# Performance work log

Hardware: AMD Instinct MI355X
Metric: run time of the kernel (lower is better)

The kernel has to match this reference:

```python
import jax, jax.numpy as jnp
import numpy as np


def setup_inputs() -> dict:
    key = jax.random.key(0)
    k1, k2, k3 = jax.random.split(key, 3)
    B, T1, T2, D = 16, 1024, 1024, 256
    x = jax.random.normal(k1, (B, T1, D), dtype=jnp.float32)
    y = jax.random.normal(k2, (B, T2, D), dtype=jnp.float32)
    WS = jax.random.normal(k3, (3 * D,), dtype=jnp.float32) * 0.05
    return {"x": x, "y": y, "WS": WS}


def reference(x, y, WS):
    # BiDAF trilinear similarity. Original computes
    #   S[b,i,j] = sum_k concat([x_i, 1, x_i])_k * concat([1, y_j, y_j])_k * WS_k
    # which decomposes exactly into:
    #   S = x @ w1 (broadcast over j) + y @ w2 (broadcast over i) + (x * w3) @ y^T
    D = x.shape[-1]
    w1, w2, w3 = WS[:D], WS[D:2 * D], WS[2 * D:]
    term_x = jnp.einsum('bid,d->bi', x, w1)            # [B, T1]
    term_y = jnp.einsum('bjd,d->bj', y, w2)            # [B, T2]
    term_xy = jnp.einsum('bid,bjd->bij', x * w3, y)    # [B, T1, T2]
    return term_xy + term_x[:, :, None] + term_y[:, None, :]
```

## Files before the change

### kernel.cpp

```cpp
#include <hip/hip_runtime.h>

#define DK 256
#define TT 1024
#define NB 16

typedef __attribute__((ext_vector_type(8))) short bf16x8;
typedef __attribute__((ext_vector_type(4))) float f32x4;

__device__ __forceinline__ unsigned int cvt_pk_bf16(float lo, float hi) {
    unsigned int r;
    asm("v_cvt_pk_bf16_f32 %0, %1, %2" : "=v"(r) : "v"(lo), "v"(hi));
    return r;
}

union BF8 { uint4 u; bf16x8 v; };

__global__ __launch_bounds__(512, 4) void fused_kernel(
    const float* __restrict__ x, const float* __restrict__ y,
    const float* __restrict__ WS, float* __restrict__ out)
{
    __shared__ unsigned short Bs[128 * DK];
    __shared__ float tys[128];

    const int tid  = threadIdx.x;
    const int lane = tid & 63;
    const int w    = tid >> 6;

    const int id = blockIdx.x;
    const int b  = id & 15;
    const int is = (id >> 4) & 3;
    const int jt = id >> 6;

    {
        const float* gY0 = y + ((size_t)b * TT + jt * 128) * DK;
        const int c = tid & 31;
        const float* w3p = WS + 2 * DK + c * 8;
        const float* w2p = WS + DK + c * 8;
        const float4 wa = *(const float4*)(w3p);
        const float4 wb = *(const float4*)(w3p + 4);
        const float4 va = *(const float4*)(w2p);
        const float4 vb = *(const float4*)(w2p + 4);
        #pragma unroll
        for (int it = 0; it < 8; ++it) {
            const int j = it * 16 + (tid >> 5);
            const float* gY = gY0 + (size_t)j * DK + c * 8;
            const float4 ya = *(const float4*)(gY);
            const float4 yb = *(const float4*)(gY + 4);
            float p = ya.x * va.x + ya.y * va.y + ya.z * va.z + ya.w * va.w
                    + yb.x * vb.x + yb.y * vb.y + yb.z * vb.z + yb.w * vb.w;
            uint4 o;
            o.x = cvt_pk_bf16(ya.x * wa.x, ya.y * wa.y);
            o.y = cvt_pk_bf16(ya.z * wa.z, ya.w * wa.w);
            o.z = cvt_pk_bf16(yb.x * wb.x, yb.y * wb.y);
            o.w = cvt_pk_bf16(yb.z * wb.z, yb.w * wb.w);
            const int slot = c ^ (j & 7);
            *(uint4*)(Bs + j * DK + slot * 8) = o;
            p += __shfl_xor(p, 1);
            p += __shfl_xor(p, 2);
            p += __shfl_xor(p, 4);
            p += __shfl_xor(p, 8);
            p += __shfl_xor(p, 16);
            if ((tid & 31) == 0) tys[j] = p;
        }
    }
    __syncthreads();

    const int mfr  = lane & 15;
    const int quad = lane >> 4;
    const int i0   = is * 256 + w * 32;
    const float* gA = x + ((size_t)b * TT + i0) * DK;

    f32x4 acc[2][8];
    #pragma unroll
    for (int it = 0; it < 2; ++it)
        #pragma unroll
        for (int n = 0; n < 8; ++n)
            acc[it][n] = (f32x4){0.f, 0.f, 0.f, 0.f};
    float txp[2] = {0.f, 0.f};

    #pragma unroll
    for (int ks = 0; ks < 8; ++ks) {
        const float* w1p = WS + ks * 32 + quad * 8;
        const float4 w1a = *(const float4*)(w1p);
        const float4 w1b = *(const float4*)(w1p + 4);
        bf16x8 av[2];
        #pragma unroll
        for (int it = 0; it < 2; ++it) {
            const float* rp = gA + (size_t)(it * 16 + mfr) * DK
                              + ks * 32 + quad * 8;
            const float4 xa = *(const float4*)rp;
            const float4 xb = *(const float4*)(rp + 4);
            txp[it] += xa.x * w1a.x + xa.y * w1a.y + xa.z * w1a.z + xa.w * w1a.w
                     + xb.x * w1b.x + xb.y * w1b.y + xb.z * w1b.z + xb.w * w1b.w;
            BF8 cv;
            cv.u.x = cvt_pk_bf16(xa.x, xa.y);
            cv.u.y = cvt_pk_bf16(xa.z, xa.w);
            cv.u.z = cvt_pk_bf16(xb.x, xb.y);
            cv.u.w = cvt_pk_bf16(xb.z, xb.w);
            av[it] = cv.v;
        }
        #pragma unroll
        for (int n = 0; n < 8; ++n) {
            const int j    = n * 16 + mfr;
            const int slot = (ks * 4 + quad) ^ (j & 7);
            const bf16x8 bv = *(const bf16x8*)(Bs + j * DK + slot * 8);
            #pragma unroll
            for (int it = 0; it < 2; ++it)
                acc[it][n] = __builtin_amdgcn_mfma_f32_16x16x32_bf16(
                    av[it], bv, acc[it][n], 0, 0, 0);
        }
    }

    #pragma unroll
    for (int it = 0; it < 2; ++it) {
        txp[it] += __shfl_xor(txp[it], 16);
        txp[it] += __shfl_xor(txp[it], 32);
    }

    float tyv[8];
    #pragma unroll
    for (int n = 0; n < 8; ++n)
        tyv[n] = tys[n * 16 + mfr];

    float* outB = out + ((size_t)b << 20) + (size_t)i0 * TT + jt * 128;
    #pragma unroll
    for (int it = 0; it < 2; ++it) {
        #pragma unroll
        for (int r = 0; r < 4; ++r) {
            const int row = it * 16 + quad * 4 + r;
            const float trow = __shfl(txp[it], (lane & 48) | (quad * 4 + r));
            #pragma unroll
            for (int n = 0; n < 8; ++n)
                outB[(size_t)row * TT + n * 16 + mfr] =
                    acc[it][n][r] + trow + tyv[n];
        }
    }
}

extern "C" void kernel_launch(void* const* d_in, const int* in_sizes, int n_in,
                              void* d_out, int out_size, void* d_ws, size_t ws_size,
                              hipStream_t stream)
{
    const float* x  = (const float*)d_in[0];
    const float* y  = (const float*)d_in[1];
    const float* WS = (const float*)d_in[2];
    float* out = (float*)d_out;
    (void)d_ws; (void)ws_size;

    fused_kernel<<<dim3(512), dim3(512), 0, stream>>>(x, y, WS, out);
}
```

Measured before the change: 109.6 us.

## Stage x tiles in LDS with double-buffered async global-to-LDS loads

Each block's 256-row x slab is now staged through a double-buffered LDS area using async global_load_lds in 32-column K slices with an XOR swizzle. The next slice is prefetched while MFMAs run on the current one, in place of direct per-lane global loads of x. This adds 64KB of LDS and a block-wide barrier per K step, and lowers the launch-bounds occupancy hint from 4 to 2. With about 128KB of LDS per block, fewer blocks can be resident per CU, which may offset the gain from the overlap.

```diff
diff --git a/kernel.cpp b/kernel.cpp
--- a/kernel.cpp
+++ b/kernel.cpp
@@ -15,11 +15,12 @@
 
 union BF8 { uint4 u; bf16x8 v; };
 
-__global__ __launch_bounds__(512, 4) void fused_kernel(
+__global__ __launch_bounds__(512, 2) void fused_kernel(
     const float* __restrict__ x, const float* __restrict__ y,
     const float* __restrict__ WS, float* __restrict__ out)
 {
     __shared__ unsigned short Bs[128 * DK];
+    __shared__ float Xp[2][256 * 32];
     __shared__ float tys[128];
 
     const int tid  = threadIdx.x;
@@ -30,6 +31,26 @@
     const int b  = id & 15;
     const int is = (id >> 4) & 3;
     const int jt = id >> 6;
+
+    const int i0blk = is * 256;
+    const float* gX = x + ((size_t)b * TT + i0blk) * DK;
+
+    const int r_ln = lane >> 3;
+    const int c_ln = lane & 7;
+
+    {
+        #pragma unroll
+        for (int t = 0; t < 4; ++t) {
+            const int q = w * 4 + t;
+            const int r = q * 8 + r_ln;
+            const int gc = c_ln ^ (r & 7);
+            const float* gp = gX + (size_t)r * DK + gc * 4;
+            float* lp = &Xp[0][q * 256];
+            __builtin_amdgcn_global_load_lds(
+                (const __attribute__((address_space(1))) void*)gp,
+                (__attribute__((address_space(3))) void*)lp, 16, 0, 0);
+        }
+    }
 
     {
         const float* gY0 = y + ((size_t)b * TT + jt * 128) * DK;
@@ -67,8 +88,8 @@
 
     const int mfr  = lane & 15;
     const int quad = lane >> 4;
-    const int i0   = is * 256 + w * 32;
-    const float* gA = x + ((size_t)b * TT + i0) * DK;
+    const int Rl0  = w * 32 + mfr;
+    const int Rl1  = Rl0 + 16;
 
     f32x4 acc[2][8];
     #pragma unroll
@@ -80,16 +101,32 @@
 
     #pragma unroll
     for (int ks = 0; ks < 8; ++ks) {
+        if (ks < 7) {
+            #pragma unroll
+            for (int t = 0; t < 4; ++t) {
+                const int q = w * 4 + t;
+                const int r = q * 8 + r_ln;
+                const int gc = c_ln ^ (r & 7);
+                const float* gp = gX + (size_t)r * DK + (ks + 1) * 32 + gc * 4;
+                float* lp = &Xp[(ks + 1) & 1][q * 256];
+                __builtin_amdgcn_global_load_lds(
+                    (const __attribute__((address_space(1))) void*)gp,
+                    (__attribute__((address_space(3))) void*)lp, 16, 0, 0);
+            }
+        }
+
         const float* w1p = WS + ks * 32 + quad * 8;
         const float4 w1a = *(const float4*)(w1p);
         const float4 w1b = *(const float4*)(w1p + 4);
         bf16x8 av[2];
+        const int Rl[2] = {Rl0, Rl1};
         #pragma unroll
         for (int it = 0; it < 2; ++it) {
-            const float* rp = gA + (size_t)(it * 16 + mfr) * DK
-                              + ks * 32 + quad * 8;
-            const float4 xa = *(const float4*)rp;
-            const float4 xb = *(const float4*)(rp + 4);
+            const float* pr = &Xp[ks & 1][Rl[it] * 32];
+            const int s0 = (quad * 2) ^ (Rl[it] & 7);
+            const int s1 = (quad * 2 + 1) ^ (Rl[it] & 7);
+            const float4 xa = *(const float4*)(pr + s0 * 4);
+            const float4 xb = *(const float4*)(pr + s1 * 4);
             txp[it] += xa.x * w1a.x + xa.y * w1a.y + xa.z * w1a.z + xa.w * w1a.w
                      + xb.x * w1b.x + xb.y * w1b.y + xb.z * w1b.z + xb.w * w1b.w;
             BF8 cv;
@@ -109,6 +146,8 @@
                 acc[it][n] = __builtin_amdgcn_mfma_f32_16x16x32_bf16(
                     av[it], bv, acc[it][n], 0, 0, 0);
         }
+
+        if (ks < 7) __syncthreads();
     }
 
     #pragma unroll
@@ -122,6 +161,7 @@
     for (int n = 0; n < 8; ++n)
         tyv[n] = tys[n * 16 + mfr];
 
+    const int i0 = i0blk + w * 32;
     float* outB = out + ((size_t)b << 20) + (size_t)i0 * TT + jt * 128;
     #pragma unroll
     for (int it = 0; it < 2; ++it) {
```

New measurement: 126.1 us. +15.1%, slower.

## Split into bf16 prep kernel and GEMM kernel reading precomputed operands

Applied to the files above, without the earlier changes.

Adds a prep kernel that converts x and y (scaled by w3) to bf16 in workspace and computes the per-row x·w1 and y·w2 projections. A separate GEMM kernel then loads bf16 operands and precomputed bias terms instead of re-reading fp32 inputs and reconverting them in every tile. The fused kernel is kept as a fallback when the workspace is too small. This trades an extra launch and a workspace write/read pass for halved operand traffic and less conversion work in the main kernel.

```diff
diff --git a/kernel.cpp b/kernel.cpp
--- a/kernel.cpp
+++ b/kernel.cpp
@@ -14,6 +14,134 @@
 }
 
 union BF8 { uint4 u; bf16x8 v; };
+
+
+__global__ __launch_bounds__(256) void prep_kernel(
+    const float* __restrict__ x, const float* __restrict__ y,
+    const float* __restrict__ WS,
+    unsigned short* __restrict__ xb, unsigned short* __restrict__ yb,
+    float* __restrict__ tx, float* __restrict__ ty)
+{
+    const int lane = threadIdx.x & 63;
+    const int gw   = blockIdx.x * 4 + (threadIdx.x >> 6);
+    const int r    = gw & 16383;
+    const bool isx = gw < 16384;
+
+    const float* src = (isx ? x : y) + (size_t)r * DK + lane * 4;
+    const float4 v  = *(const float4*)src;
+    const float4 wd = *(const float4*)(WS + (isx ? 0 : DK) + lane * 4);
+
+    float dot = v.x * wd.x + v.y * wd.y + v.z * wd.z + v.w * wd.w;
+    dot += __shfl_xor(dot, 1);
+    dot += __shfl_xor(dot, 2);
+    dot += __shfl_xor(dot, 4);
+    dot += __shfl_xor(dot, 8);
+    dot += __shfl_xor(dot, 16);
+    dot += __shfl_xor(dot, 32);
+
+    float4 s = v;
+    if (!isx) {
+        const float4 w3 = *(const float4*)(WS + 2 * DK + lane * 4);
+        s.x = v.x * w3.x; s.y = v.y * w3.y; s.z = v.z * w3.z; s.w = v.w * w3.w;
+    }
+    uint2 o;
+    o.x = cvt_pk_bf16(s.x, s.y);
+    o.y = cvt_pk_bf16(s.z, s.w);
+    unsigned short* dst = (isx ? xb : yb) + (size_t)r * DK + lane * 4;
+    *(uint2*)dst = o;
+    if (lane == 0) (isx ? tx : ty)[r] = dot;
+}
+
+__global__ __launch_bounds__(512, 4) void gemm_kernel(
+    const unsigned short* __restrict__ xb, const unsigned short* __restrict__ yb,
+    const float* __restrict__ tx, const float* __restrict__ ty,
+    float* __restrict__ out)
+{
+    __shared__ unsigned short Bs[128 * DK];
+    __shared__ float txs[256];
+    __shared__ float tys[128];
+
+    const int tid  = threadIdx.x;
+    const int lane = tid & 63;
+    const int w    = tid >> 6;
+
+    const int id = blockIdx.x;
+    const int b  = id & 15;
+    const int is = (id >> 4) & 3;
+    const int jt = id >> 6;
+
+    {
+        const unsigned short* gY = yb + ((size_t)b * TT + jt * 128) * DK;
+        #pragma unroll
+        for (int it = 0; it < 8; ++it) {
+            const int g = it * 512 + tid;
+            const int j = g >> 5;
+            const int c = g & 31;
+            const uint4 o = *(const uint4*)(gY + (size_t)j * DK + c * 8);
+            *(uint4*)(Bs + j * DK + ((c ^ (j & 7)) * 8)) = o;
+        }
+        if (tid < 64)
+            *(float4*)&txs[tid * 4] =
+                *(const float4*)(tx + b * TT + is * 256 + tid * 4);
+        else if (tid < 96)
+            *(float4*)&tys[(tid - 64) * 4] =
+                *(const float4*)(ty + b * TT + jt * 128 + (tid - 64) * 4);
+    }
+    __syncthreads();
+
+    const int mfr  = lane & 15;
+    const int quad = lane >> 4;
+    const int i0   = is * 256 + w * 32;
+    const unsigned short* gA = xb + ((size_t)b * TT + i0) * DK;
+
+    f32x4 acc[2][8];
+    #pragma unroll
+    for (int it = 0; it < 2; ++it)
+        #pragma unroll
+        for (int n = 0; n < 8; ++n)
+            acc[it][n] = (f32x4){0.f, 0.f, 0.f, 0.f};
+
+    #pragma unroll
+    for (int ks = 0; ks < 8; ++ks) {
+        bf16x8 av[2];
+        #pragma unroll
+        for (int it = 0; it < 2; ++it) {
+            BF8 cv;
+            cv.u = *(const uint4*)(gA + (size_t)(it * 16 + mfr) * DK
+                                   + ks * 32 + quad * 8);
+            av[it] = cv.v;
+        }
+        #pragma unroll
+        for (int n = 0; n < 8; ++n) {
+            const int j    = n * 16 + mfr;
+            const int slot = (ks * 4 + quad) ^ (j & 7);
+            const bf16x8 bv = *(const bf16x8*)(Bs + j * DK + slot * 8);
+            #pragma unroll
+            for (int it = 0; it < 2; ++it)
+                acc[it][n] = __builtin_amdgcn_mfma_f32_16x16x32_bf16(
+                    av[it], bv, acc[it][n], 0, 0, 0);
+        }
+    }
+
+    float tyv[8];
+    #pragma unroll
+    for (int n = 0; n < 8; ++n)
+        tyv[n] = tys[n * 16 + mfr];
+
+    float* outB = out + ((size_t)b << 20) + (size_t)i0 * TT + jt * 128;
+    #pragma unroll
+    for (int it = 0; it < 2; ++it) {
+        #pragma unroll
+        for (int r = 0; r < 4; ++r) {
+            const int row  = it * 16 + quad * 4 + r;
+            const float trow = txs[w * 32 + row];
+            #pragma unroll
+            for (int n = 0; n < 8; ++n)
+                outB[(size_t)row * TT + n * 16 + mfr] =
+                    acc[it][n][r] + trow + tyv[n];
+        }
+    }
+}
 
 __global__ __launch_bounds__(512, 4) void fused_kernel(
     const float* __restrict__ x, const float* __restrict__ y,
@@ -45,14 +173,14 @@
             const int j = it * 16 + (tid >> 5);
             const float* gY = gY0 + (size_t)j * DK + c * 8;
             const float4 ya = *(const float4*)(gY);
-            const float4 yb = *(const float4*)(gY + 4);
+            const float4 yb2 = *(const float4*)(gY + 4);
             float p = ya.x * va.x + ya.y * va.y + ya.z * va.z + ya.w * va.w
-                    + yb.x * vb.x + yb.y * vb.y + yb.z * vb.z + yb.w * vb.w;
+                    + yb2.x * vb.x + yb2.y * vb.y + yb2.z * vb.z + yb2.w * vb.w;
             uint4 o;
             o.x = cvt_pk_bf16(ya.x * wa.x, ya.y * wa.y);
             o.y = cvt_pk_bf16(ya.z * wa.z, ya.w * wa.w);
-            o.z = cvt_pk_bf16(yb.x * wb.x, yb.y * wb.y);
-            o.w = cvt_pk_bf16(yb.z * wb.z, yb.w * wb.w);
+            o.z = cvt_pk_bf16(yb2.x * wb.x, yb2.y * wb.y);
+            o.w = cvt_pk_bf16(yb2.z * wb.z, yb2.w * wb.w);
             const int slot = c ^ (j & 7);
             *(uint4*)(Bs + j * DK + slot * 8) = o;
             p += __shfl_xor(p, 1);
@@ -89,14 +217,14 @@
             const float* rp = gA + (size_t)(it * 16 + mfr) * DK
                               + ks * 32 + quad * 8;
             const float4 xa = *(const float4*)rp;
-            const float4 xb = *(const float4*)(rp + 4);
+            const float4 xb2 = *(const float4*)(rp + 4);
             txp[it] += xa.x * w1a.x + xa.y * w1a.y + xa.z * w1a.z + xa.w * w1a.w
-                     + xb.x * w1b.x + xb.y * w1b.y + xb.z * w1b.z + xb.w * w1b.w;
+                     + xb2.x * w1b.x + xb2.y * w1b.y + xb2.z * w1b.z + xb2.w * w1b.w;
             BF8 cv;
             cv.u.x = cvt_pk_bf16(xa.x, xa.y);
             cv.u.y = cvt_pk_bf16(xa.z, xa.w);
-            cv.u.z = cvt_pk_bf16(xb.x, xb.y);
-            cv.u.w = cvt_pk_bf16(xb.z, xb.w);
+            cv.u.z = cvt_pk_bf16(xb2.x, xb2.y);
+            cv.u.w = cvt_pk_bf16(xb2.z, xb2.w);
             av[it] = cv.v;
         }
         #pragma unroll
@@ -145,7 +273,21 @@
     const float* y  = (const float*)d_in[1];
     const float* WS = (const float*)d_in[2];
     float* out = (float*)d_out;
-    (void)d_ws; (void)ws_size;
-
-    fused_kernel<<<dim3(512), dim3(512), 0, stream>>>(x, y, WS, out);
-}
+
+    const size_t XB_OFF = 0;
+    const size_t YB_OFF = 8388608;
+    const size_t TX_OFF = 16777216;
+    const size_t TY_OFF = 16842752;
+    const size_t NEED   = 16908288;
+
+    if (ws_size >= NEED && d_ws != nullptr) {
+        unsigned short* xb = (unsigned short*)((char*)d_ws + XB_OFF);
+        unsigned short* yb = (unsigned short*)((char*)d_ws + YB_OFF);
+        float* tx = (float*)((char*)d_ws + TX_OFF);
+        float* ty = (float*)((char*)d_ws + TY_OFF);
+        prep_kernel<<<dim3(8192), dim3(256), 0, stream>>>(x, y, WS, xb, yb, tx, ty);
+        gemm_kernel<<<dim3(512), dim3(512), 0, stream>>>(xb, yb, tx, ty, out);
+    } else {
+        fused_kernel<<<dim3(512), dim3(512), 0, stream>>>(x, y, WS, out);
+    }
+}
```

Measured after the change: 109.0 us. Within noise of the previous version (-0.6%).
